# Performance work log

Measured on AMD Instinct MI355X. Metric: run time of the kernel, lower is better.

Reference implementation:

```python
import jax, jax.numpy as jnp
import numpy as np

B = 32768
E = 10  # number of motion experts


def _p(k, shape, scale=0.05):
    return jax.random.normal(k, shape, dtype=jnp.float32) * scale


def setup_inputs() -> dict:
    key = jax.random.key(0)
    ks = jax.random.split(key, 24)
    inp = {"input_": jax.random.normal(ks[0], (B, 556), dtype=jnp.float32)}
    # encoder 0: pose 400 -> 512 -> 512
    inp["e0_W0"] = _p(ks[1], (400, 512)); inp["e0_b0"] = jnp.zeros((512,), jnp.float32)
    inp["e0_W1"] = _p(ks[2], (512, 512)); inp["e0_b1"] = jnp.zeros((512,), jnp.float32)
    # encoder 1: goal 78 -> 128 -> 128
    inp["e1_W0"] = _p(ks[3], (78, 128)); inp["e1_b0"] = jnp.zeros((128,), jnp.float32)
    inp["e1_W1"] = _p(ks[4], (128, 128)); inp["e1_b1"] = jnp.zeros((128,), jnp.float32)
    # gating NN (1 expert => plain MLP): 78 -> 512 -> 512 -> 10, softmax
    inp["g_W0"] = _p(ks[5], (78, 512)); inp["g_b0"] = jnp.zeros((512,), jnp.float32)
    inp["g_W1"] = _p(ks[6], (512, 512)); inp["g_b1"] = jnp.zeros((512,), jnp.float32)
    inp["g_W2"] = _p(ks[7], (512, 10)); inp["g_b2"] = jnp.zeros((10,), jnp.float32)
    # motion prediction ComponentNN: 10 experts, 640 -> 512 -> 512 -> 578
    inp["m_W0"] = _p(ks[8], (E, 640, 512)); inp["m_b0"] = jnp.zeros((E, 512), jnp.float32)
    inp["m_W1"] = _p(ks[9], (E, 512, 512)); inp["m_b1"] = jnp.zeros((E, 512), jnp.float32)
    inp["m_W2"] = _p(ks[10], (E, 512, 578)); inp["m_b2"] = jnp.zeros((E, 578), jnp.float32)
    return inp


def _expert_layer(x, w, W, b):
    # sum_e w[b,e] * (x[b] @ W[e] + b[e]); blend outputs (equiv. to blending weights)
    return jnp.einsum('be,bi,eio->bo', w, x, W) + w @ b


def reference(input_, e0_W0, e0_b0, e0_W1, e0_b1, e1_W0, e1_b0, e1_W1, e1_b1,
              g_W0, g_b0, g_W1, g_b1, g_W2, g_b2,
              m_W0, m_b0, m_W1, m_b1, m_W2, m_b2):
    elu = jax.nn.elu
    pose = input_[:, 0:400]
    goal = input_[:, 400:478]
    gate_in = input_[:, 478:556]
    # encoders (dropout inactive at inference)
    h0 = elu(elu(pose @ e0_W0 + e0_b0) @ e0_W1 + e0_b1)   # [B,512]
    h1 = elu(elu(goal @ e1_W0 + e1_b0) @ e1_W1 + e1_b1)   # [B,128]
    # gating: softmax over 10 experts
    g = elu(gate_in @ g_W0 + g_b0)
    g = elu(g @ g_W1 + g_b1)
    w = jax.nn.softmax(g @ g_W2 + g_b2, axis=-1)          # [B,10]
    feat = jnp.concatenate([h0, h1], axis=-1)             # [B,640]
    x = elu(_expert_layer(feat, w, m_W0, m_b0))
    x = elu(_expert_layer(x, w, m_W1, m_b1))
    pred = _expert_layer(x, w, m_W2, m_b2)                # [B,578], linear final
    return pred
```

## Files before the change

### kernel.cpp

```cpp
#include <hip/hip_runtime.h>
#include <math.h>

typedef _Float16 h8 __attribute__((ext_vector_type(8)));
typedef float f4 __attribute__((ext_vector_type(4)));

#define BATCH 32768

__device__ __forceinline__ void gload16(const void* g, void* l) {
  __builtin_amdgcn_global_load_lds(
      (const __attribute__((address_space(1))) unsigned int*)g,
      (__attribute__((address_space(3))) unsigned int*)l, 16, 0, 0);
}

__global__ __launch_bounds__(256) void prep_input2_k(const float* __restrict__ in,
    _Float16* __restrict__ pose, _Float16* __restrict__ goal, _Float16* __restrict__ gate)
{
  const long long total = (long long)BATCH * 88;
  for (long long i = (long long)blockIdx.x * 256 + threadIdx.x; i < total;
       i += (long long)gridDim.x * 256) {
    const int b = (int)(i / 88);
    const int g = (int)(i % 88);
    const float* r = in + (size_t)b * 556;
    h8 v;
    if (g < 56) {
      const int c0 = g * 8;
      #pragma unroll
      for (int j = 0; j < 8; ++j) {
        const int c = c0 + j;
        v[j] = (_Float16)((c < 400) ? r[c] : (c == 400 ? 1.0f : 0.0f));
      }
      *reinterpret_cast<h8*>(pose + (size_t)b * 448 + c0) = v;
    } else if (g < 72) {
      const int c0 = (g - 56) * 8;
      #pragma unroll
      for (int j = 0; j < 8; ++j) {
        const int c = c0 + j;
        v[j] = (_Float16)((c < 78) ? r[400 + c] : (c == 78 ? 1.0f : 0.0f));
      }
      *reinterpret_cast<h8*>(goal + (size_t)b * 128 + c0) = v;
    } else {
      const int c0 = (g - 72) * 8;
      #pragma unroll
      for (int j = 0; j < 8; ++j) {
        const int c = c0 + j;
        v[j] = (_Float16)((c < 78) ? r[478 + c] : (c == 78 ? 1.0f : 0.0f));
      }
      *reinterpret_cast<h8*>(gate + (size_t)b * 128 + c0) = v;
    }
  }
}

__global__ __launch_bounds__(256) void prep_wt_k(const float* __restrict__ W,
    const float* __restrict__ bias, _Float16* __restrict__ out,
    int K, int N, int Nld, int Kout, int biasCols, int biasLd)
{
  __shared__ float tile[64 * 65];
  const int t = threadIdx.x;
  const int c0 = blockIdx.x * 64;
  const int n0 = blockIdx.y * 64;
  {
    const int nn = t & 63;
    #pragma unroll
    for (int i = 0; i < 16; ++i) {
      int cc = (t >> 6) + i * 4;
      int c = c0 + cc, n = n0 + nn;
      float v = 0.0f;
      if (n < N) {
        if (c < K) v = W[(size_t)c * Nld + n];
        else if (c - K < biasCols) v = bias[(size_t)(c - K) * biasLd + n];
      }
      tile[cc * 65 + nn] = v;
    }
  }
  __syncthreads();
  {
    const int cc = t & 63;
    #pragma unroll
    for (int i = 0; i < 16; ++i) {
      int nn = (t >> 6) + i * 4;
      out[(size_t)(n0 + nn) * Kout + c0 + cc] = (_Float16)tile[cc * 65 + nn];
    }
  }
}

template<bool EPI_BIAS, bool DO_ELU, bool OUT_F32>
__global__ __launch_bounds__(256, 2) void gemm_k(
    const _Float16* __restrict__ A, const _Float16* __restrict__ Bw,
    void* __restrict__ OutP, const float* __restrict__ bias,
    int ldA, int ldB, int ldO, int nChunks, int nLimit)
{
  __shared__ __align__(16) _Float16 As[2][128 * 64];
  __shared__ __align__(16) _Float16 Bs[2][128 * 64];

  const int t = threadIdx.x;
  const int m0 = blockIdx.x * 128;
  const int n0 = blockIdx.y * 128;
  const int wid = t >> 6;
  const int lane = t & 63;
  const int wm = (wid >> 1) * 64;
  const int wn = (wid & 1) * 64;
  const int lr = lane & 15;
  const int lg = lane >> 4;

  const int gr = lane >> 3;
  const int gcol = ((lane & 7) ^ gr) * 8;
  const _Float16* Abase = A + (size_t)(m0 + wid * 32 + gr) * ldA + gcol;
  const _Float16* Bbase = Bw + (size_t)(n0 + wid * 32 + gr) * ldB + gcol;

  f4 acc[4][4];
  #pragma unroll
  for (int i = 0; i < 4; ++i)
    #pragma unroll
    for (int j = 0; j < 4; ++j) { f4 z = {0.f, 0.f, 0.f, 0.f}; acc[i][j] = z; }

  auto issue = [&](int c, int buf) {
    #pragma unroll
    for (int i = 0; i < 4; ++i) {
      gload16(Abase + (size_t)(i * 8) * ldA + c * 64, &As[buf][(wid * 32 + i * 8) * 64]);
      gload16(Bbase + (size_t)(i * 8) * ldB + c * 64, &Bs[buf][(wid * 32 + i * 8) * 64]);
    }
  };

  auto mfma_step = [&](const _Float16* as, const _Float16* bs) {
    #pragma unroll
    for (int kk = 0; kk < 2; ++kk) {
      h8 af[4], bf[4];
      const int kslot = kk * 4 + lg;
      #pragma unroll
      for (int i = 0; i < 4; ++i) {
        const int row = wm + i * 16 + lr;
        af[i] = *reinterpret_cast<const h8*>(&as[row * 64 + ((kslot ^ (row & 7)) << 3)]);
      }
      #pragma unroll
      for (int j = 0; j < 4; ++j) {
        const int row = wn + j * 16 + lr;
        bf[j] = *reinterpret_cast<const h8*>(&bs[row * 64 + ((kslot ^ (row & 7)) << 3)]);
      }
      #pragma unroll
      for (int i = 0; i < 4; ++i)
        #pragma unroll
        for (int j = 0; j < 4; ++j)
          acc[i][j] = __builtin_amdgcn_mfma_f32_16x16x32_f16(af[i], bf[j], acc[i][j], 0, 0, 0);
    }
  };

  issue(0, 0);
  int cur = 0;
  for (int c = 0; c < nChunks; ++c) {
    __syncthreads();
    if (c + 1 < nChunks) issue(c + 1, cur ^ 1);
    mfma_step(As[cur], Bs[cur]);
    cur ^= 1;
  }

  #pragma unroll
  for (int j = 0; j < 4; ++j) {
    const int col = n0 + wn + j * 16 + lr;
    if (col >= nLimit) continue;
    float bvv = 0.0f;
    if (EPI_BIAS) bvv = bias[col];
    #pragma unroll
    for (int i = 0; i < 4; ++i) {
      const int rowb = m0 + wm + i * 16 + lg * 4;
      #pragma unroll
      for (int r = 0; r < 4; ++r) {
        float x = acc[i][j][r] + bvv;
        if (DO_ELU) x = (x > 0.0f) ? x : expm1f(x);
        if (OUT_F32)
          reinterpret_cast<float*>(OutP)[(size_t)(rowb + r) * ldO + col] = x;
        else
          reinterpret_cast<_Float16*>(OutP)[(size_t)(rowb + r) * ldO + col] = (_Float16)x;
      }
    }
  }
}

template<int KCe, bool DO_ELU, bool OUT_F32>
__global__ __launch_bounds__(256, 2) void expertR_k(
    const _Float16* __restrict__ A, const _Float16* __restrict__ Bw,
    void* __restrict__ OutP, const _Float16* __restrict__ wpad,
    int ldA, int ldB, int ldO, int nLimit)
{
  constexpr int E = 10;
  __shared__ __align__(16) _Float16 lds[16384 + 2560];
  _Float16* Bs = lds;
  _Float16* wT = lds + 16384;

  const int tid = threadIdx.x;
  const int w = tid >> 6;
  const int l = tid & 63;
  const int m0 = blockIdx.x * 256;
  const int n0 = blockIdx.y * 128;
  const int lr = l & 15;
  const int lg = l >> 4;

  const int strow = tid >> 3;
  const int scol = ((tid & 7) ^ (strow & 7)) * 8;

  auto stB = [&](int buf, size_t colEl) {
    _Float16* d = Bs + buf * 8192 + w * 512;
    const _Float16* s = Bw + (size_t)(n0 + strow) * ldB + colEl + scol;
    #pragma unroll
    for (int p = 0; p < 4; ++p)
      gload16(s + (size_t)(p * 32) * ldB, d + p * 2048);
  };

  auto frag = [&](const _Float16* base, int row, int kslot) -> h8 {
    return *reinterpret_cast<const h8*>(base + row * 64 + ((kslot ^ (row & 7)) << 3));
  };

  h8 araw[2][4];
  auto loadA = [&](const _Float16* base, size_t ld, size_t col0) {
    #pragma unroll
    for (int kk = 0; kk < 2; ++kk)
      #pragma unroll
      for (int mi = 0; mi < 4; ++mi)
        araw[kk][mi] = *reinterpret_cast<const h8*>(
            base + (size_t)(m0 + w * 64 + mi * 16 + lr) * ld + col0 + (size_t)(kk * 4 + lg) * 8);
  };

  f4 acc[4][8];
  #pragma unroll
  for (int mi = 0; mi < 4; ++mi)
    #pragma unroll
    for (int ni = 0; ni < 8; ++ni) { f4 z = {0.f, 0.f, 0.f, 0.f}; acc[mi][ni] = z; }

  #pragma unroll
  for (int idx = tid; idx < 2560; idx += 256) {
    const int m = idx & 255, e = idx >> 8;
    wT[e * 256 + m] = wpad[(size_t)(m0 + m) * 64 + e];
  }
  loadA(A, (size_t)ldA, 0);
  stB(0, 0);
  asm volatile("s_waitcnt vmcnt(0) lgkmcnt(0)" ::: "memory");
  __builtin_amdgcn_s_barrier();
  __builtin_amdgcn_sched_barrier(0);

  int s = 0;
  #pragma unroll 1
  for (int kc = 0; kc < KCe; ++kc) {
    #pragma unroll 1
    for (int e = 0; e < E; ++e, ++s) {
      const _Float16* Bh = Bs + (s & 1) * 8192;

      if (e + 1 < E)         stB((s + 1) & 1, (size_t)((e + 1) * KCe + kc) * 64);
      else if (kc + 1 < KCe) stB((s + 1) & 1, (size_t)(kc + 1) * 64);
      else                   stB((s + 1) & 1, (size_t)(E * KCe) * 64);
      __builtin_amdgcn_sched_barrier(0);

      _Float16 se[4];
      #pragma unroll
      for (int j = 0; j < 4; ++j) se[j] = wT[e * 256 + w * 64 + j * 16 + lr];

      #pragma unroll
      for (int kk = 0; kk < 2; ++kk) {
        h8 bf[8];
        #pragma unroll
        for (int ni = 0; ni < 8; ++ni) bf[ni] = frag(Bh, ni * 16 + lr, kk * 4 + lg);
        h8 aa[4];
        #pragma unroll
        for (int mi = 0; mi < 4; ++mi) {
          h8 v = araw[kk][mi];
          const _Float16 sv = se[mi];
          #pragma unroll
          for (int q = 0; q < 8; ++q) v[q] = v[q] * sv;
          aa[mi] = v;
        }
        __builtin_amdgcn_s_setprio(1);
        #pragma unroll
        for (int mi = 0; mi < 4; ++mi)
          #pragma unroll
          for (int ni = 0; ni < 8; ++ni)
            acc[mi][ni] = __builtin_amdgcn_mfma_f32_16x16x32_f16(aa[mi], bf[ni], acc[mi][ni], 0, 0, 0);
        __builtin_amdgcn_s_setprio(0);
      }

      __builtin_amdgcn_sched_barrier(0);
      asm volatile("s_waitcnt vmcnt(0)" ::: "memory");
      __builtin_amdgcn_s_barrier();
      __builtin_amdgcn_sched_barrier(0);
    }
    if (kc + 1 < KCe) loadA(A, (size_t)ldA, (size_t)(kc + 1) * 64);
    else              loadA(wpad, 64, 0);
  }

  {
    const _Float16* Bh = Bs + (s & 1) * 8192;
    #pragma unroll
    for (int kk = 0; kk < 2; ++kk) {
      h8 bf[8];
      #pragma unroll
      for (int ni = 0; ni < 8; ++ni) bf[ni] = frag(Bh, ni * 16 + lr, kk * 4 + lg);
      #pragma unroll
      for (int mi = 0; mi < 4; ++mi)
        #pragma unroll
        for (int ni = 0; ni < 8; ++ni)
          acc[mi][ni] = __builtin_amdgcn_mfma_f32_16x16x32_f16(araw[kk][mi], bf[ni], acc[mi][ni], 0, 0, 0);
    }
  }

  #pragma unroll
  for (int ni = 0; ni < 8; ++ni) {
    const int col = n0 + ni * 16 + lr;
    if (col >= nLimit) continue;
    #pragma unroll
    for (int mi = 0; mi < 4; ++mi) {
      const int rowb = m0 + w * 64 + mi * 16 + lg * 4;
      #pragma unroll
      for (int r = 0; r < 4; ++r) {
        float x = acc[mi][ni][r];
        if (DO_ELU) x = (x > 0.0f) ? x : expm1f(x);
        if (OUT_F32)
          reinterpret_cast<float*>(OutP)[(size_t)(rowb + r) * ldO + col] = x;
        else
          reinterpret_cast<_Float16*>(OutP)[(size_t)(rowb + r) * ldO + col] = (_Float16)x;
      }
    }
  }
}

__global__ __launch_bounds__(256) void gate_softmax_k(const _Float16* __restrict__ gb,
    const float* __restrict__ W2, const float* __restrict__ b2, _Float16* __restrict__ wpad)
{
  __shared__ float W2s[5120];
  for (int i = threadIdx.x; i < 5120; i += 256) W2s[i] = W2[i];
  __syncthreads();
  const int t = threadIdx.x;
  const int sub = t & 3;
  const int b = blockIdx.x * 64 + (t >> 2);
  const _Float16* row = gb + (size_t)b * 512 + sub * 128;
  float acc[10];
  #pragma unroll
  for (int o = 0; o < 10; ++o) acc[o] = 0.0f;
  #pragma unroll 4
  for (int k0 = 0; k0 < 128; k0 += 8) {
    h8 x = *reinterpret_cast<const h8*>(row + k0);
    #pragma unroll
    for (int jj = 0; jj < 8; ++jj) {
      float xv = (float)x[jj];
      const int k = sub * 128 + k0 + jj;
      #pragma unroll
      for (int o = 0; o < 10; ++o) acc[o] += xv * W2s[k * 10 + o];
    }
  }
  #pragma unroll
  for (int o = 0; o < 10; ++o) {
    acc[o] += __shfl_xor(acc[o], 1);
    acc[o] += __shfl_xor(acc[o], 2);
    acc[o] += b2[o];
  }
  float mx = acc[0];
  #pragma unroll
  for (int o = 1; o < 10; ++o) mx = fmaxf(mx, acc[o]);
  float s = 0.0f;
  #pragma unroll
  for (int o = 0; o < 10; ++o) { acc[o] = expf(acc[o] - mx); s += acc[o]; }
  const float inv = 1.0f / s;
  h8 o0 = {0,0,0,0,0,0,0,0}, o1 = {0,0,0,0,0,0,0,0};
  if (sub == 0) {
    #pragma unroll
    for (int o = 0; o < 8; ++o) o0[o] = (_Float16)(acc[o] * inv);
    o1[0] = (_Float16)(acc[8] * inv);
    o1[1] = (_Float16)(acc[9] * inv);
  }
  _Float16* wr = wpad + (size_t)b * 64 + sub * 16;
  *reinterpret_cast<h8*>(wr) = o0;
  *reinterpret_cast<h8*>(wr + 8) = o1;
}

extern "C" void kernel_launch(void* const* d_in, const int* in_sizes, int n_in,
                              void* d_out, int out_size, void* d_ws, size_t ws_size,
                              hipStream_t stream)
{
  const float* input_ = (const float*)d_in[0];
  const float* e0_W0 = (const float*)d_in[1];
  const float* e0_b0 = (const float*)d_in[2];
  const float* e0_W1 = (const float*)d_in[3];
  const float* e0_b1 = (const float*)d_in[4];
  const float* e1_W0 = (const float*)d_in[5];
  const float* e1_b0 = (const float*)d_in[6];
  const float* e1_W1 = (const float*)d_in[7];
  const float* e1_b1 = (const float*)d_in[8];
  const float* g_W0  = (const float*)d_in[9];
  const float* g_b0  = (const float*)d_in[10];
  const float* g_W1  = (const float*)d_in[11];
  const float* g_b1  = (const float*)d_in[12];
  const float* g_W2  = (const float*)d_in[13];
  const float* g_b2  = (const float*)d_in[14];
  const float* m_W0  = (const float*)d_in[15];
  const float* m_b0  = (const float*)d_in[16];
  const float* m_W1  = (const float*)d_in[17];
  const float* m_b1  = (const float*)d_in[18];
  const float* m_W2  = (const float*)d_in[19];
  const float* m_b2  = (const float*)d_in[20];
  (void)in_sizes; (void)n_in; (void)out_size; (void)ws_size;

  char* ws = (char*)d_ws;
  size_t off = 0;
  auto alloc = [&](size_t bytes) { char* p = ws + off; off += (bytes + 255) & ~(size_t)255; return p; };

  const size_t Bn = BATCH;
  _Float16* wsA    = (_Float16*)alloc(Bn * 512 * 2);
  _Float16* wsB    = (_Float16*)alloc(Bn * 512 * 2);
  _Float16* wsC    = (_Float16*)alloc(Bn * 640 * 2);
  _Float16* goal16 = (_Float16*)alloc(Bn * 128 * 2);
  _Float16* gate16 = (_Float16*)alloc(Bn * 128 * 2);
  _Float16* h1a16  = (_Float16*)alloc(Bn * 128 * 2);
  _Float16* wpad16 = (_Float16*)alloc(Bn * 64 * 2);
  _Float16* e0W0t  = (_Float16*)alloc((size_t)512 * 448 * 2);
  _Float16* e0W1t  = (_Float16*)alloc((size_t)512 * 512 * 2);
  _Float16* e1W0t  = (_Float16*)alloc((size_t)128 * 128 * 2);
  _Float16* e1W1t  = (_Float16*)alloc((size_t)128 * 128 * 2);
  _Float16* gW0t   = (_Float16*)alloc((size_t)512 * 128 * 2);
  _Float16* gW1t   = (_Float16*)alloc((size_t)512 * 512 * 2);
  _Float16* W0b    = (_Float16*)alloc((size_t)512 * 6464 * 2);
  _Float16* W1b    = (_Float16*)alloc((size_t)512 * 5184 * 2);
  _Float16* W2b    = (_Float16*)alloc((size_t)768 * 5184 * 2);

  dim3 blk(256);
  const int BIG = 1 << 30;

  prep_input2_k<<<dim3(2048), blk, 0, stream>>>(input_, wsA, goal16, gate16);

  prep_wt_k<<<dim3(7, 8),    blk, 0, stream>>>(e0_W0, e0_b0, e0W0t, 400, 512, 512, 448, 1, 0);
  prep_wt_k<<<dim3(8, 8),    blk, 0, stream>>>(e0_W1, nullptr, e0W1t, 512, 512, 512, 512, 0, 0);
  prep_wt_k<<<dim3(2, 2),    blk, 0, stream>>>(e1_W0, e1_b0, e1W0t, 78, 128, 128, 128, 1, 0);
  prep_wt_k<<<dim3(2, 2),    blk, 0, stream>>>(e1_W1, nullptr, e1W1t, 128, 128, 128, 128, 0, 0);
  prep_wt_k<<<dim3(2, 8),    blk, 0, stream>>>(g_W0, g_b0, gW0t, 78, 512, 512, 128, 1, 0);
  prep_wt_k<<<dim3(8, 8),    blk, 0, stream>>>(g_W1, nullptr, gW1t, 512, 512, 512, 512, 0, 0);
  prep_wt_k<<<dim3(101, 8),  blk, 0, stream>>>(m_W0, m_b0, W0b, 6400, 512, 512, 6464, 10, 512);
  prep_wt_k<<<dim3(81, 8),   blk, 0, stream>>>(m_W1, m_b1, W1b, 5120, 512, 512, 5184, 10, 512);
  prep_wt_k<<<dim3(81, 12),  blk, 0, stream>>>(m_W2, m_b2, W2b, 5120, 578, 578, 5184, 10, 578);

  gemm_k<false, true, false><<<dim3(256, 4), blk, 0, stream>>>(
      wsA, e0W0t, wsB, nullptr, 448, 448, 512, 7, BIG);
  gemm_k<true, true, false><<<dim3(256, 4), blk, 0, stream>>>(
      wsB, e0W1t, wsC, e0_b1, 512, 512, 640, 8, BIG);
  gemm_k<false, true, false><<<dim3(256, 1), blk, 0, stream>>>(
      goal16, e1W0t, h1a16, nullptr, 128, 128, 128, 2, BIG);
  gemm_k<true, true, false><<<dim3(256, 1), blk, 0, stream>>>(
      h1a16, e1W1t, wsC + 512, e1_b1, 128, 128, 640, 2, BIG);
  gemm_k<false, true, false><<<dim3(256, 4), blk, 0, stream>>>(
      gate16, gW0t, wsA, nullptr, 128, 128, 512, 2, BIG);
  gemm_k<true, true, false><<<dim3(256, 4), blk, 0, stream>>>(
      wsA, gW1t, wsB, g_b1, 512, 512, 512, 8, BIG);
  gate_softmax_k<<<dim3(BATCH / 64), blk, 0, stream>>>(wsB, g_W2, g_b2, wpad16);

  expertR_k<10, true, false><<<dim3(128, 4), blk, 0, stream>>>(
      wsC, W0b, wsA, wpad16, 640, 6464, 512, BIG);
  expertR_k<8, true, false><<<dim3(128, 4), blk, 0, stream>>>(
      wsA, W1b, wsC, wpad16, 512, 5184, 512, BIG);
  expertR_k<8, false, true><<<dim3(128, 5), blk, 0, stream>>>(
      wsC, W2b, d_out, wpad16, 512, 5184, 578, 578);
}
```

Baseline: 870.2 us.

## Triple-buffer expert weight tiles and widen final layer N tile

The expert GEMM kernel moves from double to triple buffering of weight tiles in LDS, prefetching two stages ahead. Partial vmcnt waits let loads stay in flight across the barrier. The main loop is flattened into one stage loop, with the bias stage folded in. The final layer uses a 160-column tile (NI=10), so its grid drops from 5 to 4 column blocks and less work is wasted on padding past 578. The cost is more LDS and more accumulator registers, which may lower occupancy.

```diff
diff --git a/kernel.cpp b/kernel.cpp
--- a/kernel.cpp
+++ b/kernel.cpp
@@ -175,34 +175,36 @@
   }
 }
 
-template<int KCe, bool DO_ELU, bool OUT_F32>
-__global__ __launch_bounds__(256, 2) void expertR_k(
+template<int KCe, int NI, bool DO_ELU, bool OUT_F32>
+__global__ __launch_bounds__(256, 2) void expertV_k(
     const _Float16* __restrict__ A, const _Float16* __restrict__ Bw,
     void* __restrict__ OutP, const _Float16* __restrict__ wpad,
     int ldA, int ldB, int ldO, int nLimit)
 {
   constexpr int E = 10;
-  __shared__ __align__(16) _Float16 lds[16384 + 2560];
-  _Float16* Bs = lds;
-  _Float16* wT = lds + 16384;
+  constexpr int S = KCe * E + 1;
+  constexpr int SG = NI / 2;
+  constexpr int SLOT = NI * 1024;
+  __shared__ __align__(16) _Float16 lds[3 * SLOT + 2560];
+  _Float16* wT = lds + 3 * SLOT;
 
   const int tid = threadIdx.x;
   const int w = tid >> 6;
   const int l = tid & 63;
   const int m0 = blockIdx.x * 256;
-  const int n0 = blockIdx.y * 128;
+  const int n0 = blockIdx.y * (NI * 16);
   const int lr = l & 15;
   const int lg = l >> 4;
 
   const int strow = tid >> 3;
   const int scol = ((tid & 7) ^ (strow & 7)) * 8;
 
-  auto stB = [&](int buf, size_t colEl) {
-    _Float16* d = Bs + buf * 8192 + w * 512;
-    const _Float16* s = Bw + (size_t)(n0 + strow) * ldB + colEl + scol;
-    #pragma unroll
-    for (int p = 0; p < 4; ++p)
-      gload16(s + (size_t)(p * 32) * ldB, d + p * 2048);
+  auto stB = [&](int slot, size_t colEl) {
+    _Float16* d = lds + slot * SLOT + w * 512;
+    const _Float16* sp = Bw + (size_t)(n0 + strow) * ldB + colEl + scol;
+    #pragma unroll
+    for (int p = 0; p < SG; ++p)
+      gload16(sp + (size_t)(p * 32) * ldB, d + p * 2048);
   };
 
   auto frag = [&](const _Float16* base, int row, int kslot) -> h8 {
@@ -219,11 +221,11 @@
             base + (size_t)(m0 + w * 64 + mi * 16 + lr) * ld + col0 + (size_t)(kk * 4 + lg) * 8);
   };
 
-  f4 acc[4][8];
+  f4 acc[4][NI];
   #pragma unroll
   for (int mi = 0; mi < 4; ++mi)
     #pragma unroll
-    for (int ni = 0; ni < 8; ++ni) { f4 z = {0.f, 0.f, 0.f, 0.f}; acc[mi][ni] = z; }
+    for (int ni = 0; ni < NI; ++ni) { f4 z = {0.f, 0.f, 0.f, 0.f}; acc[mi][ni] = z; }
 
   #pragma unroll
   for (int idx = tid; idx < 2560; idx += 256) {
@@ -232,75 +234,85 @@
   }
   loadA(A, (size_t)ldA, 0);
   stB(0, 0);
-  asm volatile("s_waitcnt vmcnt(0) lgkmcnt(0)" ::: "memory");
+  stB(1, (size_t)KCe * 64);
+  if constexpr (SG == 4) asm volatile("s_waitcnt vmcnt(4)" ::: "memory");
+  else                   asm volatile("s_waitcnt vmcnt(5)" ::: "memory");
+  asm volatile("s_waitcnt lgkmcnt(0)" ::: "memory");
   __builtin_amdgcn_s_barrier();
   __builtin_amdgcn_sched_barrier(0);
 
-  int s = 0;
+  int e_s = 0, kc_s = 0;
+  int e_t = 2, kc_t = 0;
   #pragma unroll 1
-  for (int kc = 0; kc < KCe; ++kc) {
-    #pragma unroll 1
-    for (int e = 0; e < E; ++e, ++s) {
-      const _Float16* Bh = Bs + (s & 1) * 8192;
-
-      if (e + 1 < E)         stB((s + 1) & 1, (size_t)((e + 1) * KCe + kc) * 64);
-      else if (kc + 1 < KCe) stB((s + 1) & 1, (size_t)(kc + 1) * 64);
-      else                   stB((s + 1) & 1, (size_t)(E * KCe) * 64);
-      __builtin_amdgcn_sched_barrier(0);
-
-      _Float16 se[4];
-      #pragma unroll
-      for (int j = 0; j < 4; ++j) se[j] = wT[e * 256 + w * 64 + j * 16 + lr];
-
-      #pragma unroll
-      for (int kk = 0; kk < 2; ++kk) {
-        h8 bf[8];
-        #pragma unroll
-        for (int ni = 0; ni < 8; ++ni) bf[ni] = frag(Bh, ni * 16 + lr, kk * 4 + lg);
-        h8 aa[4];
-        #pragma unroll
-        for (int mi = 0; mi < 4; ++mi) {
-          h8 v = araw[kk][mi];
+  for (int s = 0; s < S; ++s) {
+    const _Float16* Bh = lds + (s % 3) * SLOT;
+
+    if (s + 2 < S) {
+      const size_t col = (kc_t < KCe) ? (size_t)(e_t * KCe + kc_t) * 64
+                                      : (size_t)(E * KCe) * 64;
+      stB((s + 2) % 3, col);
+    }
+    __builtin_amdgcn_sched_barrier(0);
+
+    const bool isBias = (kc_s == KCe);
+    _Float16 se[4];
+    if (!isBias) {
+      #pragma unroll
+      for (int j = 0; j < 4; ++j) se[j] = wT[e_s * 256 + w * 64 + j * 16 + lr];
+    }
+
+    #pragma unroll
+    for (int kk = 0; kk < 2; ++kk) {
+      h8 aa[4];
+      #pragma unroll
+      for (int mi = 0; mi < 4; ++mi) {
+        h8 v = araw[kk][mi];
+        if (!isBias) {
           const _Float16 sv = se[mi];
           #pragma unroll
           for (int q = 0; q < 8; ++q) v[q] = v[q] * sv;
-          aa[mi] = v;
         }
+        aa[mi] = v;
+      }
+      #pragma unroll
+      for (int c0 = 0; c0 < NI; c0 += 4) {
+        h8 bf[4];
+        #pragma unroll
+        for (int ni = 0; ni < 4; ++ni)
+          if (c0 + ni < NI) bf[ni] = frag(Bh, (c0 + ni) * 16 + lr, kk * 4 + lg);
         __builtin_amdgcn_s_setprio(1);
         #pragma unroll
         for (int mi = 0; mi < 4; ++mi)
           #pragma unroll
-          for (int ni = 0; ni < 8; ++ni)
-            acc[mi][ni] = __builtin_amdgcn_mfma_f32_16x16x32_f16(aa[mi], bf[ni], acc[mi][ni], 0, 0, 0);
+          for (int ni = 0; ni < 4; ++ni)
+            if (c0 + ni < NI)
+              acc[mi][c0 + ni] =
+                  __builtin_amdgcn_mfma_f32_16x16x32_f16(aa[mi], bf[ni], acc[mi][c0 + ni], 0, 0, 0);
         __builtin_amdgcn_s_setprio(0);
       }
-
-      __builtin_amdgcn_sched_barrier(0);
-      asm volatile("s_waitcnt vmcnt(0)" ::: "memory");
+    }
+    __builtin_amdgcn_sched_barrier(0);
+
+    if (s + 1 < S) {
+      if (s + 2 < S) {
+        if constexpr (SG == 4) asm volatile("s_waitcnt vmcnt(4)" ::: "memory");
+        else                   asm volatile("s_waitcnt vmcnt(5)" ::: "memory");
+      } else {
+        asm volatile("s_waitcnt vmcnt(0)" ::: "memory");
+      }
       __builtin_amdgcn_s_barrier();
       __builtin_amdgcn_sched_barrier(0);
-    }
-    if (kc + 1 < KCe) loadA(A, (size_t)ldA, (size_t)(kc + 1) * 64);
-    else              loadA(wpad, 64, 0);
-  }
-
-  {
-    const _Float16* Bh = Bs + (s & 1) * 8192;
-    #pragma unroll
-    for (int kk = 0; kk < 2; ++kk) {
-      h8 bf[8];
-      #pragma unroll
-      for (int ni = 0; ni < 8; ++ni) bf[ni] = frag(Bh, ni * 16 + lr, kk * 4 + lg);
-      #pragma unroll
-      for (int mi = 0; mi < 4; ++mi)
-        #pragma unroll
-        for (int ni = 0; ni < 8; ++ni)
-          acc[mi][ni] = __builtin_amdgcn_mfma_f32_16x16x32_f16(araw[kk][mi], bf[ni], acc[mi][ni], 0, 0, 0);
-    }
-  }
-
-  #pragma unroll
-  for (int ni = 0; ni < 8; ++ni) {
+      if (e_s == E - 1) {
+        if (kc_s + 1 < KCe) loadA(A, (size_t)ldA, (size_t)(kc_s + 1) * 64);
+        else                loadA(wpad, 64, 0);
+        e_s = 0; ++kc_s;
+      } else ++e_s;
+      if (kc_t < KCe) { if (e_t == E - 1) { e_t = 0; ++kc_t; } else ++e_t; }
+    }
+  }
+
+  #pragma unroll
+  for (int ni = 0; ni < NI; ++ni) {
     const int col = n0 + ni * 16 + lr;
     if (col >= nLimit) continue;
     #pragma unroll
@@ -446,10 +458,10 @@
       wsA, gW1t, wsB, g_b1, 512, 512, 512, 8, BIG);
   gate_softmax_k<<<dim3(BATCH / 64), blk, 0, stream>>>(wsB, g_W2, g_b2, wpad16);
 
-  expertR_k<10, true, false><<<dim3(128, 4), blk, 0, stream>>>(
+  expertV_k<10, 8, true, false><<<dim3(128, 4), blk, 0, stream>>>(
       wsC, W0b, wsA, wpad16, 640, 6464, 512, BIG);
-  expertR_k<8, true, false><<<dim3(128, 4), blk, 0, stream>>>(
+  expertV_k<8, 8, true, false><<<dim3(128, 4), blk, 0, stream>>>(
       wsA, W1b, wsC, wpad16, 512, 5184, 512, BIG);
-  expertR_k<8, false, true><<<dim3(128, 5), blk, 0, stream>>>(
+  expertV_k<8, 10, false, true><<<dim3(128, 4), blk, 0, stream>>>(
       wsC, W2b, d_out, wpad16, 512, 5184, 578, 578);
 }
```

Measured after the change: 861.8 us. About the same (-1.0%).
